# Kernel optimization log

Hardware: AMD Instinct MI355X
Metric: run time of the kernel (lower is better)

## Reference

```python
import jax, jax.numpy as jnp
import numpy as np

B, C, N, D = 8, 64, 512, 64

def setup_inputs() -> dict:
    key = jax.random.key(0)
    k1, = jax.random.split(key, 1)
    inp = jax.random.normal(k1, (B, C, N, D), dtype=jnp.float32)
    a = jnp.full((1, C, 1, 1), 0.75, dtype=jnp.float32)
    b = jnp.full((1, C, 1, 1), 0.25, dtype=jnp.float32)
    return {"inp": inp, "a": a, "b": b}

def reference(inp, a, b):
    # A = inp @ inp^T : [B, C, N, N]
    A = jnp.einsum('bcnd,bcmd->bcnm', inp, inp)
    # B = A @ A : [B, C, N, N]
    B2 = jnp.einsum('bcnk,bckm->bcnm', A, A)
    Mat = -a * A + b * B2
    # out = inp + Mat @ inp : [B, C, N, D]
    out = inp + jnp.einsum('bcnm,bcmd->bcnd', Mat, inp)
    return out
```

## Files before the change

### kernel.cpp

```cpp
#include <hip/hip_runtime.h>


typedef __bf16 bf16;
typedef __attribute__((ext_vector_type(8)))  __bf16 bf16x8;
typedef __attribute__((ext_vector_type(4)))  __bf16 bf16x4;
typedef __attribute__((ext_vector_type(16))) float  f32x16;

namespace {

__device__ __forceinline__ int sxz(int d) { return ((d >> 1) ^ (d >> 4)) & 7; }

__global__ __launch_bounds__(512, 2)
void ns_mfma(const float* __restrict__ inp, const float* __restrict__ aw,
             const float* __restrict__ bw, float* __restrict__ out) {
    __shared__ unsigned char smem[72704] __attribute__((aligned(128)));
    float* const Gp  = (float*)(smem + 36864);
    bf16*  const Gbf = (bf16*)(smem + 54272);
    bf16*  const Hbf = (bf16*)(smem + 63488);
    bf16*  const Xr0 = (bf16*)smem;
    bf16*  const Xr1 = (bf16*)(smem + 18432);

    const int slice = blockIdx.x;
    const float* __restrict__ X = inp + (size_t)slice * 32768;
    float* __restrict__ O       = out + (size_t)slice * 32768;

    const int t    = threadIdx.x;
    const int lane = t & 63;
    const int w    = t >> 6;
    const int l31  = lane & 31;
    const int l5   = lane >> 5;
    const int half = t >> 8;
    const int th   = t & 255;
    const int s_nq = th >> 4;
    const int s_dq = th & 15;

    const float* __restrict__ Xbase =
        X + (size_t)(256 * (1 - half) + 4 * s_nq) * 64 + 4 * s_dq;

    bf16x4 xr[4][4];
    {
        float4 rv[4][4];
#pragma unroll
        for (int s = 0; s < 4; ++s)
#pragma unroll
            for (int rn = 0; rn < 4; ++rn)
                rv[s][rn] = *(const float4*)&Xbase[(size_t)(64 * s + rn) * 64];
#pragma unroll
        for (int s = 0; s < 4; ++s)
#pragma unroll
            for (int rn = 0; rn < 4; ++rn) {
                xr[s][rn][0] = (bf16)rv[s][rn].x;
                xr[s][rn][1] = (bf16)rv[s][rn].y;
                xr[s][rn][2] = (bf16)rv[s][rn].z;
                xr[s][rn][3] = (bf16)rv[s][rn].w;
            }
    }
    const float av = aw[slice & 63];
    const float bv = bw[slice & 63];

    f32x16 acc;
#pragma unroll
    for (int q = 0; q < 16; ++q) acc[q] = 0.f;

    const int tile = w & 3;
    const int i32  = (tile >> 1) * 32;
    const int j32  = (tile & 1) * 32;
    const int rowA = i32 + l31;
    const int rowB = j32 + l31;
    const int sA   = sxz(rowA);
    const int sB   = sxz(rowB);

    unsigned char* const XtH = smem + half * 18432;

#pragma unroll
    for (int it = 0; it < 4; ++it) {
        bf16* const Xt = (bf16*)(XtH + (it & 1) * 9216);
#pragma unroll
        for (int r = 0; r < 4; ++r) {
            const int d = 4 * s_dq + r;
            bf16x4 v;
            v[0] = xr[it][0][r]; v[1] = xr[it][1][r];
            v[2] = xr[it][2][r]; v[3] = xr[it][3][r];
            const int g = ((s_nq >> 1) ^ sxz(d)) & 7;
            *(bf16x4*)&Xt[d * 72 + g * 8 + 4 * (s_nq & 1)] = v;
        }
        __syncthreads();
#pragma unroll
        for (int ks = 0; ks < 4; ++ks) {
            const int gw = 2 * ks + l5;
            bf16x8 a = *(const bf16x8*)&Xt[rowA * 72 + ((gw ^ sA) & 7) * 8];
            bf16x8 b = *(const bf16x8*)&Xt[rowB * 72 + ((gw ^ sB) & 7) * 8];
            acc = __builtin_amdgcn_mfma_f32_32x32x16_bf16(a, b, acc, 0, 0, 0);
        }
    }
    __syncthreads();

    if (half == 0) {
#pragma unroll
        for (int q = 0; q < 16; ++q) {
            const int r = (q & 3) + 8 * (q >> 2) + 4 * l5;
            Gp[(i32 + r) * 68 + j32 + l31] = acc[q];
        }
    } else {
#pragma unroll
        for (int s = 0; s < 4; ++s) {
            bf16* const Xr = (s >> 1) ? Xr1 : Xr0;
            const int rowbase = 64 * (s & 1) + 4 * s_nq;
#pragma unroll
            for (int rn = 0; rn < 4; ++rn)
                *(bf16x4*)&Xr[(rowbase + rn) * 72 + 4 * s_dq] = xr[s][rn];
        }
    }
    __syncthreads();
    if (half == 1) {
#pragma unroll
        for (int q = 0; q < 16; ++q) {
            const int r  = (q & 3) + 8 * (q >> 2) + 4 * l5;
            const int ii = i32 + r;
            const int jj = j32 + l31;
            Gbf[ii * 72 + jj] = (bf16)(acc[q] + Gp[ii * 68 + jj]);
        }
    }
    __syncthreads();

    if (w < 4) {
        const int pi = (w >> 1) * 32;
        const int pj = (w & 1) * 32;
        f32x16 h;
#pragma unroll
        for (int q = 0; q < 16; ++q) h[q] = 0.f;
#pragma unroll
        for (int ks = 0; ks < 4; ++ks) {
            bf16x8 a = *(const bf16x8*)&Gbf[(pi + l31) * 72 + ks * 16 + 8 * l5];
            bf16x8 b = *(const bf16x8*)&Gbf[(pj + l31) * 72 + ks * 16 + 8 * l5];
            h = __builtin_amdgcn_mfma_f32_32x32x16_bf16(a, b, h, 0, 0, 0);
        }
#pragma unroll
        for (int q = 0; q < 16; ++q) {
            const int r  = (q & 3) + 8 * (q >> 2) + 4 * l5;
            const int ii = pi + r;
            const int jj = pj + l31;
            Hbf[ii * 72 + jj] = (bf16)(bv * h[q] - av * (float)Gbf[ii * 72 + jj]);
        }
    }
    __syncthreads();

    const int nb = (w >> 1) * 32;
    const int db = (w & 1) * 32;

#pragma unroll
    for (int tt = 0; tt < 4; ++tt) {
        if (tt > 0) __syncthreads();
        if (half == 0 && (tt == 1 || tt == 2)) {
            bf16* const Xr = ((tt + 1) & 1) ? Xr1 : Xr0;
#pragma unroll
            for (int ss = 0; ss < 2; ++ss) {
                const int s       = 2 * (tt - 1) + ss;
                const int rowbase = 64 * ss + 4 * s_nq;
#pragma unroll
                for (int rn = 0; rn < 4; ++rn)
                    *(bf16x4*)&Xr[(rowbase + rn) * 72 + 4 * s_dq] = xr[s][rn];
            }
        }
        const bf16* const Xr = (tt & 1) ? Xr1 : Xr0;

        f32x16 o;
#pragma unroll
        for (int q = 0; q < 16; ++q) o[q] = 0.f;
#pragma unroll
        for (int ks = 0; ks < 4; ++ks) {
            bf16x8 a = *(const bf16x8*)&Xr [(nb + l31) * 72 + ks * 16 + 8 * l5];
            bf16x8 b = *(const bf16x8*)&Hbf[(db + l31) * 72 + ks * 16 + 8 * l5];
            o = __builtin_amdgcn_mfma_f32_32x32x16_bf16(a, b, o, 0, 0, 0);
        }
#pragma unroll
        for (int q = 0; q < 16; ++q) {
            const int rl = (q & 3) + 8 * (q >> 2) + 4 * l5;
            const int nl = nb + rl;
            const int d  = db + l31;
            O[(size_t)(tt * 128 + nl) * 64 + d] = o[q] + (float)Xr[nl * 72 + d];
        }
    }
}

}

extern "C" void kernel_launch(void* const* d_in, const int* in_sizes, int n_in,
                              void* d_out, int out_size, void* d_ws, size_t ws_size,
                              hipStream_t stream) {
    const float* inp = (const float*)d_in[0];
    const float* aw  = (const float*)d_in[1];
    const float* bw  = (const float*)d_in[2];
    float* out       = (float*)d_out;

    ns_mfma<<<dim3(512), dim3(512), 0, stream>>>(inp, aw, bw, out);
}
```

Baseline: 25.40 us.

## Swizzle all LDS tiles and transpose final MFMA for vectorized float4 stores

Applies the XOR swizzle used for the Gram stage to every LDS buffer (Xr, Gbf, Hbf), aiming to cut LDS bank conflicts on the bf16x8 MFMA operand reads. The final product swaps its A/B operands so each lane holds four consecutive d values of one row, which allows float4 global stores and bf16x4 residual reads in place of scalar strided accesses. This adds some index arithmetic, and the layout change must stay consistent between every writer and reader.

```diff
diff --git a/kernel.cpp b/kernel.cpp
--- a/kernel.cpp
+++ b/kernel.cpp
@@ -9,6 +9,10 @@
 namespace {
 
 __device__ __forceinline__ int sxz(int d) { return ((d >> 1) ^ (d >> 4)) & 7; }
+
+__device__ __forceinline__ int rsw(int row, int g) {
+    return row * 72 + ((g ^ sxz(row)) & 7) * 8;
+}
 
 __global__ __launch_bounds__(512, 2)
 void ns_mfma(const float* __restrict__ inp, const float* __restrict__ aw,
@@ -67,8 +71,6 @@
     const int j32  = (tile & 1) * 32;
     const int rowA = i32 + l31;
     const int rowB = j32 + l31;
-    const int sA   = sxz(rowA);
-    const int sB   = sxz(rowB);
 
     unsigned char* const XtH = smem + half * 18432;
 
@@ -81,15 +83,13 @@
             bf16x4 v;
             v[0] = xr[it][0][r]; v[1] = xr[it][1][r];
             v[2] = xr[it][2][r]; v[3] = xr[it][3][r];
-            const int g = ((s_nq >> 1) ^ sxz(d)) & 7;
-            *(bf16x4*)&Xt[d * 72 + g * 8 + 4 * (s_nq & 1)] = v;
+            *(bf16x4*)&Xt[rsw(d, s_nq >> 1) + 4 * (s_nq & 1)] = v;
         }
         __syncthreads();
 #pragma unroll
         for (int ks = 0; ks < 4; ++ks) {
-            const int gw = 2 * ks + l5;
-            bf16x8 a = *(const bf16x8*)&Xt[rowA * 72 + ((gw ^ sA) & 7) * 8];
-            bf16x8 b = *(const bf16x8*)&Xt[rowB * 72 + ((gw ^ sB) & 7) * 8];
+            bf16x8 a = *(const bf16x8*)&Xt[rsw(rowA, 2 * ks + l5)];
+            bf16x8 b = *(const bf16x8*)&Xt[rsw(rowB, 2 * ks + l5)];
             acc = __builtin_amdgcn_mfma_f32_32x32x16_bf16(a, b, acc, 0, 0, 0);
         }
     }
@@ -108,7 +108,7 @@
             const int rowbase = 64 * (s & 1) + 4 * s_nq;
 #pragma unroll
             for (int rn = 0; rn < 4; ++rn)
-                *(bf16x4*)&Xr[(rowbase + rn) * 72 + 4 * s_dq] = xr[s][rn];
+                *(bf16x4*)&Xr[rsw(rowbase + rn, s_dq >> 1) + 4 * (s_dq & 1)] = xr[s][rn];
         }
     }
     __syncthreads();
@@ -118,7 +118,7 @@
             const int r  = (q & 3) + 8 * (q >> 2) + 4 * l5;
             const int ii = i32 + r;
             const int jj = j32 + l31;
-            Gbf[ii * 72 + jj] = (bf16)(acc[q] + Gp[ii * 68 + jj]);
+            Gbf[rsw(ii, jj >> 3) + (jj & 7)] = (bf16)(acc[q] + Gp[ii * 68 + jj]);
         }
     }
     __syncthreads();
@@ -131,8 +131,8 @@
         for (int q = 0; q < 16; ++q) h[q] = 0.f;
 #pragma unroll
         for (int ks = 0; ks < 4; ++ks) {
-            bf16x8 a = *(const bf16x8*)&Gbf[(pi + l31) * 72 + ks * 16 + 8 * l5];
-            bf16x8 b = *(const bf16x8*)&Gbf[(pj + l31) * 72 + ks * 16 + 8 * l5];
+            bf16x8 a = *(const bf16x8*)&Gbf[rsw(pi + l31, 2 * ks + l5)];
+            bf16x8 b = *(const bf16x8*)&Gbf[rsw(pj + l31, 2 * ks + l5)];
             h = __builtin_amdgcn_mfma_f32_32x32x16_bf16(a, b, h, 0, 0, 0);
         }
 #pragma unroll
@@ -140,7 +140,8 @@
             const int r  = (q & 3) + 8 * (q >> 2) + 4 * l5;
             const int ii = pi + r;
             const int jj = pj + l31;
-            Hbf[ii * 72 + jj] = (bf16)(bv * h[q] - av * (float)Gbf[ii * 72 + jj]);
+            const int o8 = rsw(ii, jj >> 3) + (jj & 7);
+            Hbf[o8] = (bf16)(bv * h[q] - av * (float)Gbf[o8]);
         }
     }
     __syncthreads();
@@ -159,7 +160,7 @@
                 const int rowbase = 64 * ss + 4 * s_nq;
 #pragma unroll
                 for (int rn = 0; rn < 4; ++rn)
-                    *(bf16x4*)&Xr[(rowbase + rn) * 72 + 4 * s_dq] = xr[s][rn];
+                    *(bf16x4*)&Xr[rsw(rowbase + rn, s_dq >> 1) + 4 * (s_dq & 1)] = xr[s][rn];
             }
         }
         const bf16* const Xr = (tt & 1) ? Xr1 : Xr0;
@@ -169,16 +170,24 @@
         for (int q = 0; q < 16; ++q) o[q] = 0.f;
 #pragma unroll
         for (int ks = 0; ks < 4; ++ks) {
-            bf16x8 a = *(const bf16x8*)&Xr [(nb + l31) * 72 + ks * 16 + 8 * l5];
-            bf16x8 b = *(const bf16x8*)&Hbf[(db + l31) * 72 + ks * 16 + 8 * l5];
+            bf16x8 a = *(const bf16x8*)&Hbf[rsw(db + l31, 2 * ks + l5)];
+            bf16x8 b = *(const bf16x8*)&Xr [rsw(nb + l31, 2 * ks + l5)];
             o = __builtin_amdgcn_mfma_f32_32x32x16_bf16(a, b, o, 0, 0, 0);
         }
-#pragma unroll
-        for (int q = 0; q < 16; ++q) {
-            const int rl = (q & 3) + 8 * (q >> 2) + 4 * l5;
-            const int nl = nb + rl;
-            const int d  = db + l31;
-            O[(size_t)(tt * 128 + nl) * 64 + d] = o[q] + (float)Xr[nl * 72 + d];
+        {
+            const int n = nb + l31;
+            float* const orow = &O[(size_t)(tt * 128 + n) * 64];
+#pragma unroll
+            for (int qg = 0; qg < 4; ++qg) {
+                const int d0 = db + 8 * qg + 4 * l5;
+                const bf16x4 xv = *(const bf16x4*)&Xr[rsw(n, d0 >> 3) + (d0 & 7)];
+                float4 ov;
+                ov.x = o[4 * qg + 0] + (float)xv[0];
+                ov.y = o[4 * qg + 1] + (float)xv[1];
+                ov.z = o[4 * qg + 2] + (float)xv[2];
+                ov.w = o[4 * qg + 3] + (float)xv[3];
+                *(float4*)&orow[d0] = ov;
+            }
         }
     }
 }
```

Result: slower. 36.24 us (+42.7%).
